# Kernel tuning notes

Measured on AMD Instinct MI355X. Metric: run time of the kernel, lower is better.

The kernel has to match this reference:

```python
import jax, jax.numpy as jnp
import numpy as np

MARGIN = 0.1
REDUCTION = 'mean'  # 'mean' or 'sum'

def setup_inputs() -> dict:
    key = jax.random.key(0)
    k1, k2 = jax.random.split(key)
    B, N = 16384, 64
    scores = jax.random.normal(k1, (B * N,), dtype=jnp.float32)
    werRank = jax.random.randint(k2, (B, N), 0, N, dtype=jnp.int64)
    return {"scores": scores, "werRank": werRank, "n_best": N}

def reference(scores, werRank, n_best):
    B = werRank.shape[0]
    N = n_best
    s = scores.reshape(B, N)                      # [B, N] per-utterance n-best scores
    g = jnp.take_along_axis(s, werRank, axis=1)   # [B, N] scores ordered by WER rank (best first)
    # pairwise margin: d[b, i, j] = g[b, j] - g[b, i] + margin, for worse-ranked j > i
    d = g[:, None, :] - g[:, :, None] + MARGIN    # [B, N, N]
    upper = jnp.triu(jnp.ones((N, N), dtype=bool), k=1)  # j > i
    hinge = jnp.where(upper[None], jnp.maximum(d, 0.0), 0.0)
    per_i = hinge.sum(axis=2)                     # [B, N] sum over worse hypotheses j
    if REDUCTION == 'mean':
        counts = (N - 1) - jnp.arange(N)          # len(nBestRank[i+1:]) for each i
        denom = jnp.where(counts > 0, counts, 1).astype(per_i.dtype)
        per_i = per_i / denom[None, :]            # row i=N-1 contributes 0 (skipped in original)
    return per_i.sum()
```

## Files before the change

### kernel.cpp

```cpp
#include <hip/hip_runtime.h>

#define MARGIN 0.1f
#define NBEST 64
#define RPW 4

__global__ __launch_bounds__(256)
void sml_kernel(const float* __restrict__ scores,
                const unsigned int* __restrict__ wr32,
                float* __restrict__ ws, int B)
{
    const int lane = threadIdx.x & 63;
    const int wib  = threadIdx.x >> 6;
    const int b0   = (blockIdx.x * 4 + wib) * RPW;

    unsigned int probe = wr32[2 * lane + 1];
    const bool is64 = (__all(probe == 0u) != 0);

    unsigned int rk[RPW];
    #pragma unroll
    for (int r = 0; r < RPW; ++r) {
        int bc = min(b0 + r, B - 1);
        rk[r] = is64 ? wr32[2 * (bc * NBEST + lane)] : wr32[bc * NBEST + lane];
    }
    float gv[RPW];
    #pragma unroll
    for (int r = 0; r < RPW; ++r) {
        int bc = min(b0 + r, B - 1);
        gv[r] = scores[bc * NBEST + (int)(rk[r] & (NBEST - 1))];
    }

    __shared__ float4 q4[4][NBEST];
    q4[wib][lane] = make_float4(gv[0] + MARGIN, gv[1] + MARGIN,
                                gv[2] + MARGIN, gv[3] + MARGIN);

    float a0 = 0.0f, a1 = 0.0f, a2 = 0.0f, a3 = 0.0f;

    __syncthreads();

    #pragma unroll
    for (int c = 1; c < NBEST; ++c) {
        float4 qa = q4[wib][c];
        float mm = (lane < c) ? 1.0f : 0.0f;
        a0 = fmaf(fmaxf(qa.x, gv[0]), mm, a0);
        a1 = fmaf(fmaxf(qa.y, gv[1]), mm, a1);
        a2 = fmaf(fmaxf(qa.z, gv[2]), mm, a2);
        a3 = fmaf(fmaxf(qa.w, gv[3]), mm, a3);
    }

    const float cntf = (float)((NBEST - 1) - lane);
    float accs = 0.0f;
    accs += (b0 + 0 < B) ? fmaf(-gv[0], cntf, a0) : 0.0f;
    accs += (b0 + 1 < B) ? fmaf(-gv[1], cntf, a1) : 0.0f;
    accs += (b0 + 2 < B) ? fmaf(-gv[2], cntf, a2) : 0.0f;
    accs += (b0 + 3 < B) ? fmaf(-gv[3], cntf, a3) : 0.0f;
    int cnt = (NBEST - 1) - lane;
    float accv = accs / (float)(cnt > 0 ? cnt : 1);

    #pragma unroll
    for (int off = 32; off > 0; off >>= 1)
        accv += __shfl_down(accv, off);

    __shared__ float wsum[4];
    if (lane == 0) wsum[wib] = accv;
    __syncthreads();
    if (threadIdx.x == 0)
        ws[blockIdx.x] = wsum[0] + wsum[1] + wsum[2] + wsum[3];
}

__global__ __launch_bounds__(256)
void sml_reduce(const float* __restrict__ ws, float* __restrict__ out, int n)
{
    const int lane = threadIdx.x & 63;
    const int wid  = threadIdx.x >> 6;
    float s = 0.0f;
    for (int i = threadIdx.x; i < n; i += 256) s += ws[i];
    #pragma unroll
    for (int off = 32; off > 0; off >>= 1)
        s += __shfl_down(s, off);
    __shared__ float wsum[4];
    if (lane == 0) wsum[wid] = s;
    __syncthreads();
    if (threadIdx.x == 0)
        out[0] = wsum[0] + wsum[1] + wsum[2] + wsum[3];
}

extern "C" void kernel_launch(void* const* d_in, const int* in_sizes, int n_in,
                              void* d_out, int out_size, void* d_ws, size_t ws_size,
                              hipStream_t stream)
{
    const float* scores    = (const float*)d_in[0];
    const unsigned int* wr = (const unsigned int*)d_in[1];
    const int B = in_sizes[0] / NBEST;

    const int rows_per_block = 4 * RPW;
    const int blocks = (B + rows_per_block - 1) / rows_per_block;
    sml_kernel<<<blocks, 256, 0, stream>>>(scores, wr, (float*)d_ws, B);
    sml_reduce<<<1, 256, 0, stream>>>((const float*)d_ws, (float*)d_out, blocks);
}
```

Before: 14.93 us.

## Replace second reduce kernel with in-kernel two-level atomic cascade

```diff
diff --git a/kernel.cpp b/kernel.cpp
--- a/kernel.cpp
+++ b/kernel.cpp
@@ -4,10 +4,12 @@
 #define NBEST 64
 #define RPW 4
 
+
 __global__ __launch_bounds__(256)
 void sml_kernel(const float* __restrict__ scores,
                 const unsigned int* __restrict__ wr32,
-                float* __restrict__ ws, int B)
+                float* __restrict__ ws, float* __restrict__ out,
+                int B, int gper )
 {
     const int lane = threadIdx.x & 63;
     const int wib  = threadIdx.x >> 6;
@@ -63,8 +65,32 @@
     __shared__ float wsum[4];
     if (lane == 0) wsum[wib] = accv;
     __syncthreads();
-    if (threadIdx.x == 0)
-        ws[blockIdx.x] = wsum[0] + wsum[1] + wsum[2] + wsum[3];
+    if (threadIdx.x != 0) return;
+    float part = wsum[0] + wsum[1] + wsum[2] + wsum[3];
+
+    if (gper == 0) { ws[16384 + blockIdx.x] = part; return; }
+
+    char* base = (char*)ws;
+    const unsigned g = (unsigned)blockIdx.x & 63u;
+    float*        slot = (float*)(base + (size_t)g * 64);
+    unsigned int* c1   = (unsigned int*)(base + 4096 + (size_t)g * 64);
+    float*        s2   = (float*)(base + 8192);
+    unsigned int* c2   = (unsigned int*)(base + 8196);
+
+    atomicAdd(slot, part);
+    __threadfence();
+    unsigned o1 = atomicAdd(c1, 1u);
+    if (o1 + 1u != (unsigned)gper) return;
+
+    __threadfence();
+    float gsum = atomicExch(slot, 0.0f);
+    atomicAdd(s2, gsum);
+    __threadfence();
+    unsigned o2 = atomicAdd(c2, 1u);
+    if (o2 + 1u != 64u) return;
+
+    __threadfence();
+    out[0] = atomicExch(s2, 0.0f);
 }
 
 __global__ __launch_bounds__(256)
@@ -73,7 +99,7 @@
     const int lane = threadIdx.x & 63;
     const int wid  = threadIdx.x >> 6;
     float s = 0.0f;
-    for (int i = threadIdx.x; i < n; i += 256) s += ws[i];
+    for (int i = threadIdx.x; i < n; i += 256) s += ws[i + 16384];
     #pragma unroll
     for (int off = 32; off > 0; off >>= 1)
         s += __shfl_down(s, off);
@@ -94,6 +120,16 @@
 
     const int rows_per_block = 4 * RPW;
     const int blocks = (B + rows_per_block - 1) / rows_per_block;
-    sml_kernel<<<blocks, 256, 0, stream>>>(scores, wr, (float*)d_ws, B);
-    sml_reduce<<<1, 256, 0, stream>>>((const float*)d_ws, (float*)d_out, blocks);
+    const bool cascade = (blocks % 64 == 0) && (ws_size >= 16384);
+
+    if (cascade) {
+        hipMemsetAsync(d_ws, 0, 8448, stream);
+        sml_kernel<<<blocks, 256, 0, stream>>>(scores, wr, (float*)d_ws,
+                                               (float*)d_out, B, blocks / 64);
+    } else {
+        sml_kernel<<<blocks, 256, 0, stream>>>(scores, wr, (float*)d_ws,
+                                               (float*)d_out, B, 0);
+        sml_reduce<<<1, 256, 0, stream>>>((const float*)d_ws, (float*)d_out,
+                                          blocks);
+    }
 }
```

Measured after the change: 31.07 us. +108.0%, slower.
